# Kernel optimization log

Hardware: AMD Instinct MI355X
Metric: run time of the kernel (lower is better)

## Reference

```python
import jax, jax.numpy as jnp
import numpy as np

N, E = 100000, 600000
IN, H = 164, 128
NH = 4  # attention heads over embed_dim H//4 = 32


def layer_norm(x, g, b, eps=1e-5):
    m = x.mean(-1, keepdims=True)
    v = x.var(-1, keepdims=True)
    return (x - m) * jax.lax.rsqrt(v + eps) * g + b


def gcn_conv(x, W, b, src, dst, n):
    # PyG GCNConv: add self-loops, symmetric D^{-1/2}(A+I)D^{-1/2} normalization.
    deg = jnp.ones((n,), x.dtype).at[dst].add(1.0)  # degree of A+I on target nodes
    dinv = jax.lax.rsqrt(deg)
    xw = x @ W  # [n, out]
    msg = xw[src] * (dinv[src] * dinv[dst])[:, None]  # gather + edge-norm
    agg = jax.ops.segment_sum(msg, dst, num_segments=n)  # scatter-add
    agg = agg + xw * (dinv * dinv)[:, None]  # self-loop term
    return agg + b


def mha_seq1(x, Wq, bq, Wk, bk, Wv, bv, Wo, bo):
    # nn.MultiheadAttention with seq_len==1: softmax over a single key -> weights==1.
    dh = x.shape[-1] // NH
    q = (x @ Wq + bq).reshape(-1, NH, dh)
    k = (x @ Wk + bk).reshape(-1, NH, dh)
    v = (x @ Wv + bv).reshape(-1, NH, dh)
    scores = jnp.sum(q * k, -1, keepdims=True) / jnp.sqrt(jnp.float32(dh))  # [n,NH,1]
    attn = jax.nn.softmax(scores[..., None], axis=-1)[..., 0]  # all ones, kept for fidelity
    out = (attn * v).reshape(-1, NH * dh)
    return out @ Wo + bo


def setup_inputs() -> dict:
    key = jax.random.key(0)
    ks = jax.random.split(key, 16)

    def kaiming(k, i, o):
        return jax.random.normal(k, (i, o), jnp.float32) * (2.0 / i) ** 0.5

    Ha, Hb, Hc = H, H // 2, H // 4  # 128, 64, 32
    return {
        "x": jax.random.normal(ks[0], (N, IN), jnp.float32),
        "edge_index": jax.random.randint(ks[1], (2, E), 0, N),
        "Wi": kaiming(ks[2], IN, Ha), "bi": jnp.zeros((Ha,), jnp.float32),
        "g1": jnp.ones((Ha,), jnp.float32), "b1": jnp.zeros((Ha,), jnp.float32),
        "Wg1": kaiming(ks[3], Ha, Ha), "bg1": jnp.zeros((Ha,), jnp.float32),
        "Wg2": kaiming(ks[4], Ha, Hb), "bg2": jnp.zeros((Hb,), jnp.float32),
        "g2": jnp.ones((Hb,), jnp.float32), "b2": jnp.zeros((Hb,), jnp.float32),
        "Wg3": kaiming(ks[5], Hb, Hc), "bg3": jnp.zeros((Hc,), jnp.float32),
        "Wq": kaiming(ks[6], Hc, Hc), "bq": jnp.zeros((Hc,), jnp.float32),
        "Wk": kaiming(ks[7], Hc, Hc), "bk": jnp.zeros((Hc,), jnp.float32),
        "Wv": kaiming(ks[8], Hc, Hc), "bv": jnp.zeros((Hc,), jnp.float32),
        "Wo": kaiming(ks[9], Hc, Hc), "bo": jnp.zeros((Hc,), jnp.float32),
        "Wc1": kaiming(ks[10], Hc, H // 8), "bc1": jnp.zeros((H // 8,), jnp.float32),
        "Wc2": kaiming(ks[11], H // 8, 32), "bc2": jnp.zeros((32,), jnp.float32),
        "Wc3": kaiming(ks[12], 32, 1), "bc3": jnp.zeros((1,), jnp.float32),
    }


def reference(x, edge_index, Wi, bi, g1, b1, Wg1, bg1, Wg2, bg2, g2, b2,
              Wg3, bg3, Wq, bq, Wk, bk, Wv, bv, Wo, bo,
              Wc1, bc1, Wc2, bc2, Wc3, bc3):
    src, dst = edge_index[0], edge_index[1]
    n = x.shape[0]
    # dropout layers are identity in eval mode
    h = layer_norm(jax.nn.relu(x @ Wi + bi), g1, b1)
    h1 = jax.nn.relu(gcn_conv(h, Wg1, bg1, src, dst, n)) + h
    h2 = layer_norm(jax.nn.relu(gcn_conv(h1, Wg2, bg2, src, dst, n)), g2, b2)
    h3 = jax.nn.relu(gcn_conv(h2, Wg3, bg3, src, dst, n))
    h3 = mha_seq1(h3, Wq, bq, Wk, bk, Wv, bv, Wo, bo)
    h3 = jax.nn.relu(h3 @ Wc1 + bc1)
    h3 = jax.nn.relu(h3 @ Wc2 + bc2)
    return (h3 @ Wc3 + bc3)[:, 0]
```

## Files before the change

kernel.cpp:

```cpp
#include <hip/hip_runtime.h>


typedef __attribute__((ext_vector_type(8))) _Float16 f16x8;
typedef __attribute__((ext_vector_type(4))) _Float16 f16x4;
typedef __attribute__((ext_vector_type(4))) float f32x4;

#define GLOAD_LDS16(gp, lp)                                        \
  __builtin_amdgcn_global_load_lds(                                \
      (const __attribute__((address_space(1))) void*)(gp),         \
      (__attribute__((address_space(3))) void*)(lp), 16, 0, 0)

static __device__ __forceinline__ void wait_vm0() {
  asm volatile("s_waitcnt vmcnt(0)" ::: "memory");
}
static __device__ __forceinline__ void wait_vm1() {
  asm volatile("s_waitcnt vmcnt(1)" ::: "memory");
}
static __device__ __forceinline__ void wait_vm2() {
  asm volatile("s_waitcnt vmcnt(2)" ::: "memory");
}

__global__ void k_count(const int* __restrict__ dst, int* __restrict__ counts, int e) {
  int i = blockIdx.x * blockDim.x + threadIdx.x;
  if (i < e) atomicAdd(&counts[dst[i]], 1);
}

__global__ __launch_bounds__(256) void k_scan_part(
    const int* __restrict__ counts, int* __restrict__ bsums, int n) {
  int tid = threadIdx.x;
  int i0 = blockIdx.x * 1024 + tid * 4;
  int s = 0;
#pragma unroll
  for (int k = 0; k < 4; k++) { int i = i0 + k; if (i < n) s += counts[i]; }
#pragma unroll
  for (int d = 1; d < 64; d <<= 1) s += __shfl_xor(s, d);
  __shared__ int wsum[4];
  int lane = tid & 63, w = tid >> 6;
  if (lane == 0) wsum[w] = s;
  __syncthreads();
  if (tid == 0) bsums[blockIdx.x] = wsum[0] + wsum[1] + wsum[2] + wsum[3];
}

__global__ __launch_bounds__(128) void k_scan_top(int* __restrict__ bsums, int nb) {
  int tid = threadIdx.x;
  int orig = (tid < nb) ? bsums[tid] : 0;
  int v = orig;
  int lane = tid & 63, w = tid >> 6;
#pragma unroll
  for (int d = 1; d < 64; d <<= 1) { int t = __shfl_up(v, d); if (lane >= d) v += t; }
  __shared__ int ws[2];
  if (lane == 63) ws[w] = v;
  __syncthreads();
  if (w == 1) v += ws[0];
  if (tid < nb) bsums[tid] = v - orig;
}

__global__ __launch_bounds__(256) void k_scan_down(
    int* __restrict__ counts, const int* __restrict__ bsums,
    int* __restrict__ offsets, float* __restrict__ dinv, int n, int e) {
  int tid = threadIdx.x;
  int i0 = blockIdx.x * 1024 + tid * 4;
  int c[4]; int tsum = 0;
#pragma unroll
  for (int k = 0; k < 4; k++) { int i = i0 + k; c[k] = (i < n) ? counts[i] : 0; tsum += c[k]; }
  int v = tsum;
  int lane = tid & 63, w = tid >> 6;
#pragma unroll
  for (int d = 1; d < 64; d <<= 1) { int t = __shfl_up(v, d); if (lane >= d) v += t; }
  __shared__ int wsum[4];
  if (lane == 63) wsum[w] = v;
  __syncthreads();
  int wadd = 0;
#pragma unroll
  for (int q = 0; q < 4; q++) if (q < w) wadd += wsum[q];
  int run = (v - tsum) + wadd + bsums[blockIdx.x];
#pragma unroll
  for (int k = 0; k < 4; k++) {
    int i = i0 + k;
    if (i < n) {
      offsets[i] = run;
      dinv[i] = rsqrtf((float)(c[k] + 1));
      counts[i] = 0;
    }
    run += c[k];
  }
  if (blockIdx.x == 0 && tid == 0) offsets[n] = e;
}

__global__ void k_fill(const int* __restrict__ src, const int* __restrict__ dst,
                       const int* __restrict__ offsets, int* __restrict__ cursor,
                       const float* __restrict__ dinv, int2* __restrict__ csr, int e) {
  int i = blockIdx.x * blockDim.x + threadIdx.x;
  if (i >= e) return;
  int s = src[i], d = dst[i];
  int pos = atomicAdd(&cursor[d], 1);
  csr[offsets[d] + pos] = make_int2(s, __float_as_int(dinv[s] * dinv[d]));
}

__device__ __forceinline__ void pack_hi(const float* __restrict__ W,
                                        _Float16* __restrict__ dst,
                                        int K, int N, int u) {
  int lane = u & 63; int rest = u >> 6; int CT = N >> 4;
  int ct = rest % CT, ks = rest / CT;
  int gcol = ct * 16 + (lane & 15);
  int gk0 = ks * 32 + (lane >> 4) * 8;
  size_t o = (size_t)(ks * CT + ct) * 512 + lane * 8;
#pragma unroll
  for (int i = 0; i < 8; i++) {
    float v = (gk0 + i < K) ? W[(size_t)(gk0 + i) * N + gcol] : 0.0f;
    dst[o + i] = (_Float16)v;
  }
}

__global__ void k_setup(const float* __restrict__ Wi, const float* __restrict__ Wg1,
                        const float* __restrict__ Wg2, const float* __restrict__ Wg3,
                        _Float16* __restrict__ pWi, _Float16* __restrict__ pWg1,
                        _Float16* __restrict__ pWg2, _Float16* __restrict__ pWg3,
                        int* __restrict__ counts, float* __restrict__ zp, int n) {
  int b = blockIdx.x;
  if (b < 25) {
    int t = b * 256 + threadIdx.x;
    if (t < 3072) pack_hi(Wi, pWi, 164, 128, t);
    else if (t < 5120) pack_hi(Wg1, pWg1, 128, 128, t - 3072);
    else if (t < 6144) pack_hi(Wg2, pWg2, 128, 64, t - 5120);
    else if (t < 6400) pack_hi(Wg3, pWg3, 64, 32, t - 6144);
  } else {
    if (b == 25 && threadIdx.x < 64) zp[threadIdx.x] = 0.0f;
    int i = (b - 25) * 256 + threadIdx.x;
    if (i < n) counts[i] = 0;
  }
}

__global__ __launch_bounds__(512, 4) void k_gemm_in(
    const float* __restrict__ x, const _Float16* __restrict__ pB,
    const float* __restrict__ bias, const float* __restrict__ gamma,
    const float* __restrict__ beta, const float* __restrict__ zp,
    _Float16* __restrict__ out, int n) {
  constexpr int N = 128, CT = 8;
  __shared__ __align__(16) float sAi[8][2][512];
  int tid = threadIdx.x;
  int lane = tid & 63, w = tid >> 6;
  int rowbase = blockIdx.x * 128 + w * 16;
  const f16x8* Bf = (const f16x8*)pB;

  auto stage = [&](int ks, int buf) {
#pragma unroll
    for (int j = 0; j < 2; j++) {
      int r_ = j * 8 + (lane >> 3);
      int c_ = (lane & 7) ^ (lane >> 3);
      int rg = rowbase + r_;
      bool ok = (rg < n) && (ks < 5 || c_ == 0);
      const void* s = ok ? (const void*)(x + (size_t)rg * 164 + ks * 32 + c_ * 4)
                         : (const void*)zp;
      GLOAD_LDS16(s, &sAi[w][buf][j * 256]);
    }
  };

  f32x4 acc[CT];
#pragma unroll
  for (int c = 0; c < CT; c++) acc[c] = (f32x4)0.0f;

  int rr = lane & 15;
  int c0 = (lane >> 4) * 2;
  int s0 = c0 ^ (rr & 7);
  int s1 = (c0 + 1) ^ (rr & 7);

  stage(0, 0);
#pragma unroll
  for (int ks = 0; ks < 6; ks++) {
    f16x8 bfr[CT];
#pragma unroll
    for (int c = 0; c < CT; c++) bfr[c] = Bf[(ks * CT + c) * 64 + lane];
    if (ks + 1 < 6) { stage(ks + 1, (ks + 1) & 1); wait_vm2(); }
    else wait_vm0();
    const float* bp = &sAi[w][ks & 1][0];
    float4 u0 = *(const float4*)&bp[rr * 32 + s0 * 4];
    float4 u1 = *(const float4*)&bp[rr * 32 + s1 * 4];
    float v[8] = {u0.x, u0.y, u0.z, u0.w, u1.x, u1.y, u1.z, u1.w};
    f16x8 ah, al;
#pragma unroll
    for (int i = 0; i < 8; i++) {
      ah[i] = (_Float16)v[i];
      al[i] = (_Float16)(v[i] - (float)ah[i]);
    }
#pragma unroll
    for (int c = 0; c < CT; c++) {
      acc[c] = __builtin_amdgcn_mfma_f32_16x16x32_f16(ah, bfr[c], acc[c], 0, 0, 0);
      acc[c] = __builtin_amdgcn_mfma_f32_16x16x32_f16(al, bfr[c], acc[c], 0, 0, 0);
    }
  }

  int r0 = (lane >> 4) * 4;
  int li = lane & 15;
  float s1v[4] = {0, 0, 0, 0}, s2v[4] = {0, 0, 0, 0};
#pragma unroll
  for (int c = 0; c < CT; c++) {
    float bb = bias[c * 16 + li];
#pragma unroll
    for (int r = 0; r < 4; r++) {
      float t = acc[c][r] + bb;
      t = t > 0.0f ? t : 0.0f;
      acc[c][r] = t;
      s1v[r] += t;
      s2v[r] += t * t;
    }
  }
#pragma unroll
  for (int m = 1; m < 16; m <<= 1) {
#pragma unroll
    for (int r = 0; r < 4; r++) {
      s1v[r] += __shfl_xor(s1v[r], m);
      s2v[r] += __shfl_xor(s2v[r], m);
    }
  }
#pragma unroll
  for (int c = 0; c < CT; c++) {
    float gv = gamma[c * 16 + li], bv = beta[c * 16 + li];
#pragma unroll
    for (int r = 0; r < 4; r++) {
      int node = rowbase + r0 + r;
      if (node < n) {
        float mean = s1v[r] * (1.0f / N);
        float var = s2v[r] * (1.0f / N) - mean * mean;
        float rs = rsqrtf(var + 1e-5f);
        out[(size_t)node * N + c * 16 + li] =
            (_Float16)((acc[c][r] - mean) * rs * gv + bv);
      }
    }
  }
}

template <int K, int N>
__global__ __launch_bounds__(512, 4) void k_gemm_f16(
    const _Float16* __restrict__ A, const _Float16* __restrict__ pB,
    const float* __restrict__ zp, _Float16* __restrict__ out, int n) {
  constexpr int KS = K / 32, CT = N / 16;
  __shared__ __align__(16) _Float16 sA[8][2][512];
  int tid = threadIdx.x;
  int lane = tid & 63, w = tid >> 6;
  int rowbase = blockIdx.x * 128 + w * 16;
  const f16x8* Bf = (const f16x8*)pB;

  int r_ = lane >> 2;
  int c_ = (lane & 3) ^ (r_ & 3);
  int rg = rowbase + r_;
  const _Float16* asrc = A + (size_t)rg * K + c_ * 8;
  bool rok = rg < n;

  auto stage = [&](int ks, int buf) {
    const void* s = rok ? (const void*)(asrc + ks * 32) : (const void*)zp;
    GLOAD_LDS16(s, &sA[w][buf][0]);
  };

  f32x4 acc[CT];
#pragma unroll
  for (int c = 0; c < CT; c++) acc[c] = (f32x4)0.0f;

  int rr = lane & 15;
  int slot = (lane >> 4) ^ (rr & 3);

  stage(0, 0);
#pragma unroll
  for (int ks = 0; ks < KS; ks++) {
    f16x8 bfr[CT];
#pragma unroll
    for (int c = 0; c < CT; c++) bfr[c] = Bf[(ks * CT + c) * 64 + lane];
    if (ks + 1 < KS) { stage(ks + 1, (ks + 1) & 1); wait_vm1(); }
    else wait_vm0();
    f16x8 av = *(const f16x8*)&sA[w][ks & 1][rr * 32 + slot * 8];
#pragma unroll
    for (int c = 0; c < CT; c++) {
      acc[c] = __builtin_amdgcn_mfma_f32_16x16x32_f16(av, bfr[c], acc[c], 0, 0, 0);
    }
  }

  int r0 = (lane >> 4) * 4;
  int li = lane & 15;
#pragma unroll
  for (int c = 0; c < CT; c++) {
#pragma unroll
    for (int r = 0; r < 4; r++) {
      int node = rowbase + r0 + r;
      if (node < n) out[(size_t)node * N + c * 16 + li] = (_Float16)acc[c][r];
    }
  }
}

template <int OUT_D, int MODE>
__global__ __launch_bounds__(256, 2) void k_gather(
    const int* __restrict__ off, const int2* __restrict__ csr,
    const _Float16* __restrict__ xw, const float* __restrict__ dinv,
    const float* __restrict__ bias, const _Float16* __restrict__ auxh,
    const float* __restrict__ gamma, const float* __restrict__ beta,
    _Float16* __restrict__ out, int n) {
  constexpr int TPN = OUT_D / 4;
  constexpr int NPB = 256 / TPN;
  int tid = threadIdx.x;
  int node = blockIdx.x * NPB + tid / TPN;
  int li = tid % TPN;
  if (node >= n) return;
  int start = off[node], end = off[node + 1];
  float di = dinv[node];
  float d2 = di * di;
  const _Float16* xp = xw + 4 * li;
  f16x4 self = *(const f16x4*)(xp + (size_t)node * OUT_D);
  f16x4 hres;
  if constexpr (MODE == 0)
    hres = *(const f16x4*)(auxh + (size_t)node * OUT_D + 4 * li);
  float a0 = (float)self[0] * d2 + bias[4 * li + 0];
  float a1 = (float)self[1] * d2 + bias[4 * li + 1];
  float a2 = (float)self[2] * d2 + bias[4 * li + 2];
  float a3 = (float)self[3] * d2 + bias[4 * li + 3];
  for (int cb = start; cb < end; cb += TPN) {
    int m = end - cb; if (m > TPN) m = TPN;
    int sv = node; float nv = 0.0f;
    if (li < m) { int2 me = csr[cb + li]; sv = me.x; nv = __int_as_float(me.y); }
    for (int j0 = 0; j0 < m; j0 += 8) {
      int s0 = __shfl(sv, j0 + 0, TPN), s1 = __shfl(sv, j0 + 1, TPN);
      int s2 = __shfl(sv, j0 + 2, TPN), s3 = __shfl(sv, j0 + 3, TPN);
      int s4 = __shfl(sv, j0 + 4, TPN), s5 = __shfl(sv, j0 + 5, TPN);
      int s6 = __shfl(sv, j0 + 6, TPN), s7 = __shfl(sv, j0 + 7, TPN);
      float w0 = __shfl(nv, j0 + 0, TPN), w1 = __shfl(nv, j0 + 1, TPN);
      float w2 = __shfl(nv, j0 + 2, TPN), w3 = __shfl(nv, j0 + 3, TPN);
      float w4 = __shfl(nv, j0 + 4, TPN), w5 = __shfl(nv, j0 + 5, TPN);
      float w6 = __shfl(nv, j0 + 6, TPN), w7 = __shfl(nv, j0 + 7, TPN);
      f16x4 v0 = *(const f16x4*)(xp + (size_t)s0 * OUT_D);
      f16x4 v1 = *(const f16x4*)(xp + (size_t)s1 * OUT_D);
      f16x4 v2 = *(const f16x4*)(xp + (size_t)s2 * OUT_D);
      f16x4 v3 = *(const f16x4*)(xp + (size_t)s3 * OUT_D);
      f16x4 v4 = *(const f16x4*)(xp + (size_t)s4 * OUT_D);
      f16x4 v5 = *(const f16x4*)(xp + (size_t)s5 * OUT_D);
      f16x4 v6 = *(const f16x4*)(xp + (size_t)s6 * OUT_D);
      f16x4 v7 = *(const f16x4*)(xp + (size_t)s7 * OUT_D);
      a0 += (float)v0[0] * w0 + (float)v1[0] * w1 + (float)v2[0] * w2 + (float)v3[0] * w3
          + (float)v4[0] * w4 + (float)v5[0] * w5 + (float)v6[0] * w6 + (float)v7[0] * w7;
      a1 += (float)v0[1] * w0 + (float)v1[1] * w1 + (float)v2[1] * w2 + (float)v3[1] * w3
          + (float)v4[1] * w4 + (float)v5[1] * w5 + (float)v6[1] * w6 + (float)v7[1] * w7;
      a2 += (float)v0[2] * w0 + (float)v1[2] * w1 + (float)v2[2] * w2 + (float)v3[2] * w3
          + (float)v4[2] * w4 + (float)v5[2] * w5 + (float)v6[2] * w6 + (float)v7[2] * w7;
      a3 += (float)v0[3] * w0 + (float)v1[3] * w1 + (float)v2[3] * w2 + (float)v3[3] * w3
          + (float)v4[3] * w4 + (float)v5[3] * w5 + (float)v6[3] * w6 + (float)v7[3] * w7;
    }
  }
  _Float16* po = out + (size_t)node * OUT_D + 4 * li;
  if constexpr (MODE == 0) {
    f16x4 o;
    o[0] = (_Float16)((a0 > 0.0f ? a0 : 0.0f) + (float)hres[0]);
    o[1] = (_Float16)((a1 > 0.0f ? a1 : 0.0f) + (float)hres[1]);
    o[2] = (_Float16)((a2 > 0.0f ? a2 : 0.0f) + (float)hres[2]);
    o[3] = (_Float16)((a3 > 0.0f ? a3 : 0.0f) + (float)hres[3]);
    *(f16x4*)po = o;
  } else if constexpr (MODE == 1) {
    float v0 = a0 > 0.0f ? a0 : 0.0f, v1 = a1 > 0.0f ? a1 : 0.0f;
    float v2 = a2 > 0.0f ? a2 : 0.0f, v3 = a3 > 0.0f ? a3 : 0.0f;
    float s1 = v0 + v1 + v2 + v3;
    float s2 = v0 * v0 + v1 * v1 + v2 * v2 + v3 * v3;
#pragma unroll
    for (int d = 1; d < TPN; d <<= 1) {
      s1 += __shfl_xor(s1, d, TPN);
      s2 += __shfl_xor(s2, d, TPN);
    }
    float m_ = s1 * (1.0f / OUT_D);
    float var = s2 * (1.0f / OUT_D) - m_ * m_;
    float rs = rsqrtf(var + 1e-5f);
    f16x4 o;
    o[0] = (_Float16)((v0 - m_) * rs * gamma[4 * li + 0] + beta[4 * li + 0]);
    o[1] = (_Float16)((v1 - m_) * rs * gamma[4 * li + 1] + beta[4 * li + 1]);
    o[2] = (_Float16)((v2 - m_) * rs * gamma[4 * li + 2] + beta[4 * li + 2]);
    o[3] = (_Float16)((v3 - m_) * rs * gamma[4 * li + 3] + beta[4 * li + 3]);
    *(f16x4*)po = o;
  } else {
    f16x4 o;
    o[0] = (_Float16)a0; o[1] = (_Float16)a1;
    o[2] = (_Float16)a2; o[3] = (_Float16)a3;
    *(f16x4*)po = o;
  }
}

__global__ __launch_bounds__(256) void k_tail(
    const _Float16* __restrict__ agg3, const float* __restrict__ Wv,
    const float* __restrict__ bv, const float* __restrict__ Wo,
    const float* __restrict__ bo, const float* __restrict__ Wc1,
    const float* __restrict__ bc1, const float* __restrict__ Wc2,
    const float* __restrict__ bc2, const float* __restrict__ Wc3,
    const float* __restrict__ bc3, float* __restrict__ out, int n) {
  __shared__ float sWv[1024], sWo[1024], sWc1[512], sWc2[512];
  __shared__ float sbv[32], sbo[32], sbc2[32], sWc3[32], sbc1[16], sbc3[1];
  int tid = threadIdx.x;
  for (int i = tid; i < 1024; i += 256) { sWv[i] = Wv[i]; sWo[i] = Wo[i]; }
  for (int i = tid; i < 512; i += 256) { sWc1[i] = Wc1[i]; sWc2[i] = Wc2[i]; }
  if (tid < 32) { sbv[tid] = bv[tid]; sbo[tid] = bo[tid];
                  sbc2[tid] = bc2[tid]; sWc3[tid] = Wc3[tid]; }
  if (tid < 16) sbc1[tid] = bc1[tid];
  if (tid == 0) sbc3[0] = bc3[0];
  __syncthreads();
  int node = blockIdx.x * blockDim.x + tid;
  if (node >= n) return;
  float a[32];
  const f16x8* row8 = (const f16x8*)(agg3 + (size_t)node * 32);
#pragma unroll
  for (int q = 0; q < 4; q++) {
    f16x8 t = row8[q];
#pragma unroll
    for (int i = 0; i < 8; i++) {
      float f = (float)t[i];
      a[8 * q + i] = f > 0.0f ? f : 0.0f;
    }
  }
  float v[32];
#pragma unroll
  for (int j = 0; j < 32; j++) v[j] = sbv[j];
  for (int k = 0; k < 32; k++) {
#pragma unroll
    for (int j = 0; j < 32; j++) v[j] += a[k] * sWv[k * 32 + j];
  }
  float o[32];
#pragma unroll
  for (int j = 0; j < 32; j++) o[j] = sbo[j];
  for (int k = 0; k < 32; k++) {
#pragma unroll
    for (int j = 0; j < 32; j++) o[j] += v[k] * sWo[k * 32 + j];
  }
  float c1[16];
#pragma unroll
  for (int j = 0; j < 16; j++) c1[j] = sbc1[j];
  for (int k = 0; k < 32; k++) {
#pragma unroll
    for (int j = 0; j < 16; j++) c1[j] += o[k] * sWc1[k * 16 + j];
  }
#pragma unroll
  for (int j = 0; j < 16; j++) c1[j] = c1[j] > 0.0f ? c1[j] : 0.0f;
  float c2[32];
#pragma unroll
  for (int j = 0; j < 32; j++) c2[j] = sbc2[j];
  for (int k = 0; k < 16; k++) {
#pragma unroll
    for (int j = 0; j < 32; j++) c2[j] += c1[k] * sWc2[k * 32 + j];
  }
  float r = sbc3[0];
#pragma unroll
  for (int k = 0; k < 32; k++) {
    float c = c2[k] > 0.0f ? c2[k] : 0.0f;
    r += c * sWc3[k];
  }
  out[node] = r;
}

extern "C" void kernel_launch(void* const* d_in, const int* in_sizes, int n_in,
                              void* d_out, int out_size, void* d_ws, size_t ws_size,
                              hipStream_t stream) {
  const float* x   = (const float*)d_in[0];
  const int* ei    = (const int*)d_in[1];
  const float* Wi  = (const float*)d_in[2];
  const float* bi  = (const float*)d_in[3];
  const float* g1  = (const float*)d_in[4];
  const float* b1  = (const float*)d_in[5];
  const float* Wg1 = (const float*)d_in[6];
  const float* bg1 = (const float*)d_in[7];
  const float* Wg2 = (const float*)d_in[8];
  const float* bg2 = (const float*)d_in[9];
  const float* g2  = (const float*)d_in[10];
  const float* b2  = (const float*)d_in[11];
  const float* Wg3 = (const float*)d_in[12];
  const float* bg3 = (const float*)d_in[13];
  const float* Wv  = (const float*)d_in[18];
  const float* bv  = (const float*)d_in[19];
  const float* Wo  = (const float*)d_in[20];
  const float* bo  = (const float*)d_in[21];
  const float* Wc1 = (const float*)d_in[22];
  const float* bc1 = (const float*)d_in[23];
  const float* Wc2 = (const float*)d_in[24];
  const float* bc2 = (const float*)d_in[25];
  const float* Wc3 = (const float*)d_in[26];
  const float* bc3 = (const float*)d_in[27];

  const int n = in_sizes[0] / 164;
  const int e = in_sizes[1] / 2;
  const int* src = ei;
  const int* dst = ei + e;

  char* ws = (char*)d_ws;
  size_t off = 0;
  auto alloc = [&](size_t bytes) {
    char* p = ws + off;
    off += (bytes + 255) & ~(size_t)255;
    return p;
  };
  _Float16* A     = (_Float16*)alloc((size_t)n * 128 * 2);
  _Float16* B     = (_Float16*)alloc((size_t)n * 128 * 2);
  _Float16* C     = (_Float16*)alloc((size_t)n * 128 * 2);
  float* dinv     = (float*)alloc((size_t)n * 4);
  int*   counts   = (int*)alloc((size_t)n * 4);
  int*   offsets  = (int*)alloc((size_t)(n + 1) * 4);
  int*   bsums    = (int*)alloc(128 * 4);
  int2*  csr      = (int2*)alloc((size_t)e * 8);
  _Float16* pWi   = (_Float16*)alloc(3072 * 16);
  _Float16* pWg1  = (_Float16*)alloc(2048 * 16);
  _Float16* pWg2  = (_Float16*)alloc(1024 * 16);
  _Float16* pWg3  = (_Float16*)alloc(256 * 16);
  float* zp       = (float*)alloc(64 * 4);
  (void)ws_size;

  const int BS = 256;
  const int SB = (n + 1023) / 1024;
  const int GB = (n + 127) / 128;

  k_setup<<<25 + (n + 255) / 256, 256, 0, stream>>>(
      Wi, Wg1, Wg2, Wg3, pWi, pWg1, pWg2, pWg3, counts, zp, n);

  k_count<<<(e + BS - 1) / BS, BS, 0, stream>>>(dst, counts, e);
  k_scan_part<<<SB, 256, 0, stream>>>(counts, bsums, n);
  k_scan_top<<<1, 128, 0, stream>>>(bsums, SB);
  k_scan_down<<<SB, 256, 0, stream>>>(counts, bsums, offsets, dinv, n, e);
  k_fill<<<(e + BS - 1) / BS, BS, 0, stream>>>(src, dst, offsets, counts, dinv,
                                               csr, e);

  k_gemm_in<<<GB, 512, 0, stream>>>(x, pWi, bi, g1, b1, zp, A, n);

  k_gemm_f16<128, 128><<<GB, 512, 0, stream>>>(A, pWg1, zp, B, n);
  k_gather<128, 0><<<(n + 7) / 8, 256, 0, stream>>>(
      offsets, csr, B, dinv, bg1, A, nullptr, nullptr, C, n);

  k_gemm_f16<128, 64><<<GB, 512, 0, stream>>>(C, pWg2, zp, A, n);
  k_gather<64, 1><<<(n + 15) / 16, 256, 0, stream>>>(
      offsets, csr, A, dinv, bg2, nullptr, g2, b2, B, n);

  k_gemm_f16<64, 32><<<GB, 512, 0, stream>>>(B, pWg3, zp, A, n);
  k_gather<32, 2><<<(n + 31) / 32, 256, 0, stream>>>(
      offsets, csr, A, dinv, bg3, nullptr, nullptr, nullptr, C, n);

  k_tail<<<(n + BS - 1) / BS, BS, 0, stream>>>(
      C, Wv, bv, Wo, bo, Wc1, bc1, Wc2, bc2, Wc3, bc3, (float*)d_out, n);
}
```

Baseline: 227.4 us.

## Fuse final gather into tail, merge scan stages, stage GEMM outputs via LDS, drop split-f16

Several changes at once. The final GCN gather is fused into the MLP tail kernel through an LDS tile, which removes one launch and the f16 round trip of the aggregated features. The top-level scan kernel is dropped, and each scan_down block now sums its own prefix of block sums. The GEMM epilogues are staged through LDS so global stores become coalesced 16-byte writes. The input GEMM also drops the hi/lo f16 split, which halves its MFMAs but lowers input precision to plain f16.

```diff
diff --git a/kernel.cpp b/kernel.cpp
--- a/kernel.cpp
+++ b/kernel.cpp
@@ -18,6 +18,10 @@
 }
 static __device__ __forceinline__ void wait_vm2() {
   asm volatile("s_waitcnt vmcnt(2)" ::: "memory");
+}
+static __device__ __forceinline__ void wait_lgkm0() {
+  asm volatile("s_waitcnt lgkmcnt(0)" ::: "memory");
+  __builtin_amdgcn_sched_barrier(0);
 }
 
 __global__ void k_count(const int* __restrict__ dst, int* __restrict__ counts, int e) {
@@ -41,39 +45,32 @@
   if (tid == 0) bsums[blockIdx.x] = wsum[0] + wsum[1] + wsum[2] + wsum[3];
 }
 
-__global__ __launch_bounds__(128) void k_scan_top(int* __restrict__ bsums, int nb) {
-  int tid = threadIdx.x;
-  int orig = (tid < nb) ? bsums[tid] : 0;
-  int v = orig;
-  int lane = tid & 63, w = tid >> 6;
-#pragma unroll
-  for (int d = 1; d < 64; d <<= 1) { int t = __shfl_up(v, d); if (lane >= d) v += t; }
-  __shared__ int ws[2];
-  if (lane == 63) ws[w] = v;
-  __syncthreads();
-  if (w == 1) v += ws[0];
-  if (tid < nb) bsums[tid] = v - orig;
-}
-
 __global__ __launch_bounds__(256) void k_scan_down(
     int* __restrict__ counts, const int* __restrict__ bsums,
-    int* __restrict__ offsets, float* __restrict__ dinv, int n, int e) {
+    int* __restrict__ offsets, float* __restrict__ dinv, int n, int e, int nb) {
   int tid = threadIdx.x;
+  int lane = tid & 63, w = tid >> 6;
+  __shared__ int wsum[4], psum[4];
+  int pv = (tid < nb && tid < blockIdx.x) ? bsums[tid] : 0;
+#pragma unroll
+  for (int d = 1; d < 64; d <<= 1) pv += __shfl_xor(pv, d);
+  if (lane == 0) psum[w] = pv;
+  __syncthreads();
+  int blockpref = psum[0] + psum[1] + psum[2] + psum[3];
+
   int i0 = blockIdx.x * 1024 + tid * 4;
   int c[4]; int tsum = 0;
 #pragma unroll
   for (int k = 0; k < 4; k++) { int i = i0 + k; c[k] = (i < n) ? counts[i] : 0; tsum += c[k]; }
   int v = tsum;
-  int lane = tid & 63, w = tid >> 6;
 #pragma unroll
   for (int d = 1; d < 64; d <<= 1) { int t = __shfl_up(v, d); if (lane >= d) v += t; }
-  __shared__ int wsum[4];
   if (lane == 63) wsum[w] = v;
   __syncthreads();
   int wadd = 0;
 #pragma unroll
   for (int q = 0; q < 4; q++) if (q < w) wadd += wsum[q];
-  int run = (v - tsum) + wadd + bsums[blockIdx.x];
+  int run = (v - tsum) + wadd + blockpref;
 #pragma unroll
   for (int k = 0; k < 4; k++) {
     int i = i0 + k;
@@ -177,17 +174,12 @@
     float4 u0 = *(const float4*)&bp[rr * 32 + s0 * 4];
     float4 u1 = *(const float4*)&bp[rr * 32 + s1 * 4];
     float v[8] = {u0.x, u0.y, u0.z, u0.w, u1.x, u1.y, u1.z, u1.w};
-    f16x8 ah, al;
-#pragma unroll
-    for (int i = 0; i < 8; i++) {
-      ah[i] = (_Float16)v[i];
-      al[i] = (_Float16)(v[i] - (float)ah[i]);
-    }
-#pragma unroll
-    for (int c = 0; c < CT; c++) {
+    f16x8 ah;
+#pragma unroll
+    for (int i = 0; i < 8; i++) ah[i] = (_Float16)v[i];
+#pragma unroll
+    for (int c = 0; c < CT; c++)
       acc[c] = __builtin_amdgcn_mfma_f32_16x16x32_f16(ah, bfr[c], acc[c], 0, 0, 0);
-      acc[c] = __builtin_amdgcn_mfma_f32_16x16x32_f16(al, bfr[c], acc[c], 0, 0, 0);
-    }
   }
 
   int r0 = (lane >> 4) * 4;
@@ -213,20 +205,29 @@
       s2v[r] += __shfl_xor(s2v[r], m);
     }
   }
+  wait_lgkm0();
+  _Float16* lr = (_Float16*)&sAi[w][0][0];
 #pragma unroll
   for (int c = 0; c < CT; c++) {
     float gv = gamma[c * 16 + li], bv = beta[c * 16 + li];
 #pragma unroll
     for (int r = 0; r < 4; r++) {
-      int node = rowbase + r0 + r;
-      if (node < n) {
-        float mean = s1v[r] * (1.0f / N);
-        float var = s2v[r] * (1.0f / N) - mean * mean;
-        float rs = rsqrtf(var + 1e-5f);
-        out[(size_t)node * N + c * 16 + li] =
-            (_Float16)((acc[c][r] - mean) * rs * gv + bv);
-      }
-    }
+      float mean = s1v[r] * (1.0f / N);
+      float var = s2v[r] * (1.0f / N) - mean * mean;
+      float rs = rsqrtf(var + 1e-5f);
+      lr[(r0 + r) * 128 + c * 16 + li] =
+          (_Float16)((acc[c][r] - mean) * rs * gv + bv);
+    }
+  }
+  wait_lgkm0();
+#pragma unroll
+  for (int i = 0; i < 4; i++) {
+    int chunk = i * 64 + lane;
+    int rloc = chunk >> 4;
+    int cc = chunk & 15;
+    if (rowbase + rloc < n)
+      *(f16x8*)&out[(size_t)(rowbase + rloc) * 128 + cc * 8] =
+          *(const f16x8*)&lr[chunk * 8];
   }
 }
 
@@ -236,6 +237,7 @@
     const float* __restrict__ zp, _Float16* __restrict__ out, int n) {
   constexpr int KS = K / 32, CT = N / 16;
   __shared__ __align__(16) _Float16 sA[8][2][512];
+  __shared__ __align__(16) _Float16 sR[8][16 * N];
   int tid = threadIdx.x;
   int lane = tid & 63, w = tid >> 6;
   int rowbase = blockIdx.x * 128 + w * 16;
@@ -269,20 +271,29 @@
     else wait_vm0();
     f16x8 av = *(const f16x8*)&sA[w][ks & 1][rr * 32 + slot * 8];
 #pragma unroll
-    for (int c = 0; c < CT; c++) {
+    for (int c = 0; c < CT; c++)
       acc[c] = __builtin_amdgcn_mfma_f32_16x16x32_f16(av, bfr[c], acc[c], 0, 0, 0);
-    }
   }
 
   int r0 = (lane >> 4) * 4;
   int li = lane & 15;
+  wait_lgkm0();
+  _Float16* lr = &sR[w][0];
 #pragma unroll
   for (int c = 0; c < CT; c++) {
 #pragma unroll
-    for (int r = 0; r < 4; r++) {
-      int node = rowbase + r0 + r;
-      if (node < n) out[(size_t)node * N + c * 16 + li] = (_Float16)acc[c][r];
-    }
+    for (int r = 0; r < 4; r++)
+      lr[(r0 + r) * N + c * 16 + li] = (_Float16)acc[c][r];
+  }
+  wait_lgkm0();
+#pragma unroll
+  for (int i = 0; i < N / 32; i++) {
+    int chunk = i * 64 + lane;
+    int rloc = chunk / (N / 8);
+    int cc = chunk % (N / 8);
+    if (rowbase + rloc < n)
+      *(f16x8*)&out[(size_t)(rowbase + rloc) * N + cc * 8] =
+          *(const f16x8*)&lr[chunk * 8];
   }
 }
 
@@ -350,7 +361,7 @@
     o[2] = (_Float16)((a2 > 0.0f ? a2 : 0.0f) + (float)hres[2]);
     o[3] = (_Float16)((a3 > 0.0f ? a3 : 0.0f) + (float)hres[3]);
     *(f16x4*)po = o;
-  } else if constexpr (MODE == 1) {
+  } else {
     float v0 = a0 > 0.0f ? a0 : 0.0f, v1 = a1 > 0.0f ? a1 : 0.0f;
     float v2 = a2 > 0.0f ? a2 : 0.0f, v3 = a3 > 0.0f ? a3 : 0.0f;
     float s1 = v0 + v1 + v2 + v3;
@@ -369,21 +380,19 @@
     o[2] = (_Float16)((v2 - m_) * rs * gamma[4 * li + 2] + beta[4 * li + 2]);
     o[3] = (_Float16)((v3 - m_) * rs * gamma[4 * li + 3] + beta[4 * li + 3]);
     *(f16x4*)po = o;
-  } else {
-    f16x4 o;
-    o[0] = (_Float16)a0; o[1] = (_Float16)a1;
-    o[2] = (_Float16)a2; o[3] = (_Float16)a3;
-    *(f16x4*)po = o;
-  }
-}
-
-__global__ __launch_bounds__(256) void k_tail(
-    const _Float16* __restrict__ agg3, const float* __restrict__ Wv,
+  }
+}
+
+__global__ __launch_bounds__(256, 2) void k_gt(
+    const int* __restrict__ off, const int2* __restrict__ csr,
+    const _Float16* __restrict__ xw, const float* __restrict__ dinv,
+    const float* __restrict__ bg3, const float* __restrict__ Wv,
     const float* __restrict__ bv, const float* __restrict__ Wo,
     const float* __restrict__ bo, const float* __restrict__ Wc1,
     const float* __restrict__ bc1, const float* __restrict__ Wc2,
     const float* __restrict__ bc2, const float* __restrict__ Wc3,
     const float* __restrict__ bc3, float* __restrict__ out, int n) {
+  __shared__ float sAgg[256][33];
   __shared__ float sWv[1024], sWo[1024], sWc1[512], sWc2[512];
   __shared__ float sbv[32], sbo[32], sbc2[32], sWc3[32], sbc1[16], sbc3[1];
   int tid = threadIdx.x;
@@ -393,19 +402,65 @@
                   sbc2[tid] = bc2[tid]; sWc3[tid] = Wc3[tid]; }
   if (tid < 16) sbc1[tid] = bc1[tid];
   if (tid == 0) sbc3[0] = bc3[0];
+
+  int base0 = blockIdx.x * 256;
+  int li = tid & 7;
+  const _Float16* xp = xw + 4 * li;
+  for (int sub = 0; sub < 8; sub++) {
+    int nl = sub * 32 + (tid >> 3);
+    int node = base0 + nl;
+    if (node < n) {
+      int start = off[node], end = off[node + 1];
+      float di = dinv[node];
+      float d2 = di * di;
+      f16x4 self = *(const f16x4*)(xp + (size_t)node * 32);
+      float a0 = (float)self[0] * d2 + bg3[4 * li + 0];
+      float a1 = (float)self[1] * d2 + bg3[4 * li + 1];
+      float a2 = (float)self[2] * d2 + bg3[4 * li + 2];
+      float a3 = (float)self[3] * d2 + bg3[4 * li + 3];
+      for (int cb = start; cb < end; cb += 8) {
+        int m = end - cb; if (m > 8) m = 8;
+        int sv = node; float nv = 0.0f;
+        if (li < m) { int2 me = csr[cb + li]; sv = me.x; nv = __int_as_float(me.y); }
+        for (int j0 = 0; j0 < m; j0 += 8) {
+          int s0 = __shfl(sv, j0 + 0, 8), s1 = __shfl(sv, j0 + 1, 8);
+          int s2 = __shfl(sv, j0 + 2, 8), s3 = __shfl(sv, j0 + 3, 8);
+          int s4 = __shfl(sv, j0 + 4, 8), s5 = __shfl(sv, j0 + 5, 8);
+          int s6 = __shfl(sv, j0 + 6, 8), s7 = __shfl(sv, j0 + 7, 8);
+          float w0 = __shfl(nv, j0 + 0, 8), w1 = __shfl(nv, j0 + 1, 8);
+          float w2 = __shfl(nv, j0 + 2, 8), w3 = __shfl(nv, j0 + 3, 8);
+          float w4 = __shfl(nv, j0 + 4, 8), w5 = __shfl(nv, j0 + 5, 8);
+          float w6 = __shfl(nv, j0 + 6, 8), w7 = __shfl(nv, j0 + 7, 8);
+          f16x4 v0 = *(const f16x4*)(xp + (size_t)s0 * 32);
+          f16x4 v1 = *(const f16x4*)(xp + (size_t)s1 * 32);
+          f16x4 v2 = *(const f16x4*)(xp + (size_t)s2 * 32);
+          f16x4 v3 = *(const f16x4*)(xp + (size_t)s3 * 32);
+          f16x4 v4 = *(const f16x4*)(xp + (size_t)s4 * 32);
+          f16x4 v5 = *(const f16x4*)(xp + (size_t)s5 * 32);
+          f16x4 v6 = *(const f16x4*)(xp + (size_t)s6 * 32);
+          f16x4 v7 = *(const f16x4*)(xp + (size_t)s7 * 32);
+          a0 += (float)v0[0] * w0 + (float)v1[0] * w1 + (float)v2[0] * w2 + (float)v3[0] * w3
+              + (float)v4[0] * w4 + (float)v5[0] * w5 + (float)v6[0] * w6 + (float)v7[0] * w7;
+          a1 += (float)v0[1] * w0 + (float)v1[1] * w1 + (float)v2[1] * w2 + (float)v3[1] * w3
+              + (float)v4[1] * w4 + (float)v5[1] * w5 + (float)v6[1] * w6 + (float)v7[1] * w7;
+          a2 += (float)v0[2] * w0 + (float)v1[2] * w1 + (float)v2[2] * w2 + (float)v3[2] * w3
+              + (float)v4[2] * w4 + (float)v5[2] * w5 + (float)v6[2] * w6 + (float)v7[2] * w7;
+          a3 += (float)v0[3] * w0 + (float)v1[3] * w1 + (float)v2[3] * w2 + (float)v3[3] * w3
+              + (float)v4[3] * w4 + (float)v5[3] * w5 + (float)v6[3] * w6 + (float)v7[3] * w7;
+        }
+      }
+      float* dst = &sAgg[nl][4 * li];
+      dst[0] = a0; dst[1] = a1; dst[2] = a2; dst[3] = a3;
+    }
+  }
   __syncthreads();
-  int node = blockIdx.x * blockDim.x + tid;
+  int node = base0 + tid;
   if (node >= n) return;
   float a[32];
-  const f16x8* row8 = (const f16x8*)(agg3 + (size_t)node * 32);
-#pragma unroll
-  for (int q = 0; q < 4; q++) {
-    f16x8 t = row8[q];
-#pragma unroll
-    for (int i = 0; i < 8; i++) {
-      float f = (float)t[i];
-      a[8 * q + i] = f > 0.0f ? f : 0.0f;
-    }
+#pragma unroll
+  for (int j = 0; j < 32; j++) {
+    float f = sAgg[tid][j];
+    a[j] = f > 0.0f ? f : 0.0f;
   }
   float v[32];
 #pragma unroll
@@ -492,7 +547,7 @@
   float* dinv     = (float*)alloc((size_t)n * 4);
   int*   counts   = (int*)alloc((size_t)n * 4);
   int*   offsets  = (int*)alloc((size_t)(n + 1) * 4);
-  int*   bsums    = (int*)alloc(128 * 4);
+  int*   bsums    = (int*)alloc(256 * 4);
   int2*  csr      = (int2*)alloc((size_t)e * 8);
   _Float16* pWi   = (_Float16*)alloc(3072 * 16);
   _Float16* pWg1  = (_Float16*)alloc(2048 * 16);
@@ -510,8 +565,7 @@
 
   k_count<<<(e + BS - 1) / BS, BS, 0, stream>>>(dst, counts, e);
   k_scan_part<<<SB, 256, 0, stream>>>(counts, bsums, n);
-  k_scan_top<<<1, 128, 0, stream>>>(bsums, SB);
-  k_scan_down<<<SB, 256, 0, stream>>>(counts, bsums, offsets, dinv, n, e);
+  k_scan_down<<<SB, 256, 0, stream>>>(counts, bsums, offsets, dinv, n, e, SB);
   k_fill<<<(e + BS - 1) / BS, BS, 0, stream>>>(src, dst, offsets, counts, dinv,
                                                csr, e);
 
@@ -526,9 +580,7 @@
       offsets, csr, A, dinv, bg2, nullptr, g2, b2, B, n);
 
   k_gemm_f16<64, 32><<<GB, 512, 0, stream>>>(B, pWg3, zp, A, n);
-  k_gather<32, 2><<<(n + 31) / 32, 256, 0, stream>>>(
-      offsets, csr, A, dinv, bg3, nullptr, nullptr, nullptr, C, n);
-
-  k_tail<<<(n + BS - 1) / BS, BS, 0, stream>>>(
-      C, Wv, bv, Wo, bo, Wc1, bc1, Wc2, bc2, Wc3, bc3, (float*)d_out, n);
-}
+  k_gt<<<(n + 255) / 256, 256, 0, stream>>>(
+      offsets, csr, A, dinv, bg3, Wv, bv, Wo, bo, Wc1, bc1, Wc2, bc2,
+      Wc3, bc3, (float*)d_out, n);
+}
```

After: 219.1 us. -3.7%, faster.

## Prefetch B fragments, stage GEMM outputs via LDS, drop split-fp16 and scan_top

Applied to the files above, without the earlier changes.

Several changes land together. The GEMM kernels now double-buffer the B weight fragments in registers, one k-step ahead, and adjust the vmcnt waits to match. Outputs are written through LDS as 16-byte row-contiguous stores instead of scattered 2-byte stores. The scan kernel is dropped: each scan_down block now sums the partial sums of the blocks before it itself. Separately, k_gemm_in stops using the hi/lo fp16 split for x, halving its MFMAs at the cost of fp32 input precision.

```diff
diff --git a/kernel.cpp b/kernel.cpp
--- a/kernel.cpp
+++ b/kernel.cpp
@@ -13,11 +13,18 @@
 static __device__ __forceinline__ void wait_vm0() {
   asm volatile("s_waitcnt vmcnt(0)" ::: "memory");
 }
-static __device__ __forceinline__ void wait_vm1() {
-  asm volatile("s_waitcnt vmcnt(1)" ::: "memory");
-}
-static __device__ __forceinline__ void wait_vm2() {
-  asm volatile("s_waitcnt vmcnt(2)" ::: "memory");
+static __device__ __forceinline__ void wait_vm10() {
+  asm volatile("s_waitcnt vmcnt(10)" ::: "memory");
+}
+static __device__ __forceinline__ void wait_vm5() {
+  asm volatile("s_waitcnt vmcnt(5)" ::: "memory");
+}
+static __device__ __forceinline__ void wait_vm3() {
+  asm volatile("s_waitcnt vmcnt(3)" ::: "memory");
+}
+static __device__ __forceinline__ void wait_lgkm0() {
+  asm volatile("s_waitcnt lgkmcnt(0)" ::: "memory");
+  __builtin_amdgcn_sched_barrier(0);
 }
 
 __global__ void k_count(const int* __restrict__ dst, int* __restrict__ counts, int e) {
@@ -41,39 +48,32 @@
   if (tid == 0) bsums[blockIdx.x] = wsum[0] + wsum[1] + wsum[2] + wsum[3];
 }
 
-__global__ __launch_bounds__(128) void k_scan_top(int* __restrict__ bsums, int nb) {
-  int tid = threadIdx.x;
-  int orig = (tid < nb) ? bsums[tid] : 0;
-  int v = orig;
-  int lane = tid & 63, w = tid >> 6;
-#pragma unroll
-  for (int d = 1; d < 64; d <<= 1) { int t = __shfl_up(v, d); if (lane >= d) v += t; }
-  __shared__ int ws[2];
-  if (lane == 63) ws[w] = v;
-  __syncthreads();
-  if (w == 1) v += ws[0];
-  if (tid < nb) bsums[tid] = v - orig;
-}
-
 __global__ __launch_bounds__(256) void k_scan_down(
     int* __restrict__ counts, const int* __restrict__ bsums,
-    int* __restrict__ offsets, float* __restrict__ dinv, int n, int e) {
+    int* __restrict__ offsets, float* __restrict__ dinv, int n, int e, int nb) {
   int tid = threadIdx.x;
+  int lane = tid & 63, w = tid >> 6;
+  __shared__ int wsum[4], psum[4];
+  int pv = (tid < nb && tid < blockIdx.x) ? bsums[tid] : 0;
+#pragma unroll
+  for (int d = 1; d < 64; d <<= 1) pv += __shfl_xor(pv, d);
+  if (lane == 0) psum[w] = pv;
+  __syncthreads();
+  int blockpref = psum[0] + psum[1] + psum[2] + psum[3];
+
   int i0 = blockIdx.x * 1024 + tid * 4;
   int c[4]; int tsum = 0;
 #pragma unroll
   for (int k = 0; k < 4; k++) { int i = i0 + k; c[k] = (i < n) ? counts[i] : 0; tsum += c[k]; }
   int v = tsum;
-  int lane = tid & 63, w = tid >> 6;
 #pragma unroll
   for (int d = 1; d < 64; d <<= 1) { int t = __shfl_up(v, d); if (lane >= d) v += t; }
-  __shared__ int wsum[4];
   if (lane == 63) wsum[w] = v;
   __syncthreads();
   int wadd = 0;
 #pragma unroll
   for (int q = 0; q < 4; q++) if (q < w) wadd += wsum[q];
-  int run = (v - tsum) + wadd + bsums[blockIdx.x];
+  int run = (v - tsum) + wadd + blockpref;
 #pragma unroll
   for (int k = 0; k < 4; k++) {
     int i = i0 + k;
@@ -136,7 +136,7 @@
     const float* __restrict__ bias, const float* __restrict__ gamma,
     const float* __restrict__ beta, const float* __restrict__ zp,
     _Float16* __restrict__ out, int n) {
-  constexpr int N = 128, CT = 8;
+  constexpr int N = 128, CT = 8, KS = 6;
   __shared__ __align__(16) float sAi[8][2][512];
   int tid = threadIdx.x;
   int lane = tid & 63, w = tid >> 6;
@@ -165,29 +165,32 @@
   int s0 = c0 ^ (rr & 7);
   int s1 = (c0 + 1) ^ (rr & 7);
 
+  f16x8 bfr[2][CT];
+#pragma unroll
+  for (int c = 0; c < CT; c++) bfr[0][c] = Bf[c * 64 + lane];
   stage(0, 0);
-#pragma unroll
-  for (int ks = 0; ks < 6; ks++) {
-    f16x8 bfr[CT];
-#pragma unroll
-    for (int c = 0; c < CT; c++) bfr[c] = Bf[(ks * CT + c) * 64 + lane];
-    if (ks + 1 < 6) { stage(ks + 1, (ks + 1) & 1); wait_vm2(); }
-    else wait_vm0();
+
+#pragma unroll
+  for (int ks = 0; ks < KS; ks++) {
+    if (ks + 1 < KS) {
+#pragma unroll
+      for (int c = 0; c < CT; c++)
+        bfr[(ks + 1) & 1][c] = Bf[((ks + 1) * CT + c) * 64 + lane];
+      stage(ks + 1, (ks + 1) & 1);
+      wait_vm10();
+    } else {
+      wait_vm0();
+    }
     const float* bp = &sAi[w][ks & 1][0];
     float4 u0 = *(const float4*)&bp[rr * 32 + s0 * 4];
     float4 u1 = *(const float4*)&bp[rr * 32 + s1 * 4];
     float v[8] = {u0.x, u0.y, u0.z, u0.w, u1.x, u1.y, u1.z, u1.w};
-    f16x8 ah, al;
-#pragma unroll
-    for (int i = 0; i < 8; i++) {
-      ah[i] = (_Float16)v[i];
-      al[i] = (_Float16)(v[i] - (float)ah[i]);
-    }
-#pragma unroll
-    for (int c = 0; c < CT; c++) {
-      acc[c] = __builtin_amdgcn_mfma_f32_16x16x32_f16(ah, bfr[c], acc[c], 0, 0, 0);
-      acc[c] = __builtin_amdgcn_mfma_f32_16x16x32_f16(al, bfr[c], acc[c], 0, 0, 0);
-    }
+    f16x8 ah;
+#pragma unroll
+    for (int i = 0; i < 8; i++) ah[i] = (_Float16)v[i];
+#pragma unroll
+    for (int c = 0; c < CT; c++)
+      acc[c] = __builtin_amdgcn_mfma_f32_16x16x32_f16(ah, bfr[ks & 1][c], acc[c], 0, 0, 0);
   }
 
   int r0 = (lane >> 4) * 4;
@@ -213,20 +216,29 @@
       s2v[r] += __shfl_xor(s2v[r], m);
     }
   }
+  wait_lgkm0();
+  _Float16* lr = (_Float16*)&sAi[w][0][0];
 #pragma unroll
   for (int c = 0; c < CT; c++) {
     float gv = gamma[c * 16 + li], bv = beta[c * 16 + li];
 #pragma unroll
     for (int r = 0; r < 4; r++) {
-      int node = rowbase + r0 + r;
-      if (node < n) {
-        float mean = s1v[r] * (1.0f / N);
-        float var = s2v[r] * (1.0f / N) - mean * mean;
-        float rs = rsqrtf(var + 1e-5f);
-        out[(size_t)node * N + c * 16 + li] =
-            (_Float16)((acc[c][r] - mean) * rs * gv + bv);
-      }
-    }
+      float mean = s1v[r] * (1.0f / N);
+      float var = s2v[r] * (1.0f / N) - mean * mean;
+      float rs = rsqrtf(var + 1e-5f);
+      lr[(r0 + r) * 128 + c * 16 + li] =
+          (_Float16)((acc[c][r] - mean) * rs * gv + bv);
+    }
+  }
+  wait_lgkm0();
+#pragma unroll
+  for (int i = 0; i < 4; i++) {
+    int chunk = i * 64 + lane;
+    int rloc = chunk >> 4;
+    int cc = chunk & 15;
+    if (rowbase + rloc < n)
+      *(f16x8*)&out[(size_t)(rowbase + rloc) * 128 + cc * 8] =
+          *(const f16x8*)&lr[chunk * 8];
   }
 }
 
@@ -236,6 +248,7 @@
     const float* __restrict__ zp, _Float16* __restrict__ out, int n) {
   constexpr int KS = K / 32, CT = N / 16;
   __shared__ __align__(16) _Float16 sA[8][2][512];
+  __shared__ __align__(16) _Float16 sR[8][16 * N];
   int tid = threadIdx.x;
   int lane = tid & 63, w = tid >> 6;
   int rowbase = blockIdx.x * 128 + w * 16;
@@ -259,30 +272,47 @@
   int rr = lane & 15;
   int slot = (lane >> 4) ^ (rr & 3);
 
+  f16x8 bfr[2][CT];
+#pragma unroll
+  for (int c = 0; c < CT; c++) bfr[0][c] = Bf[c * 64 + lane];
   stage(0, 0);
+
 #pragma unroll
   for (int ks = 0; ks < KS; ks++) {
-    f16x8 bfr[CT];
-#pragma unroll
-    for (int c = 0; c < CT; c++) bfr[c] = Bf[(ks * CT + c) * 64 + lane];
-    if (ks + 1 < KS) { stage(ks + 1, (ks + 1) & 1); wait_vm1(); }
-    else wait_vm0();
+    if (ks + 1 < KS) {
+#pragma unroll
+      for (int c = 0; c < CT; c++)
+        bfr[(ks + 1) & 1][c] = Bf[((ks + 1) * CT + c) * 64 + lane];
+      stage(ks + 1, (ks + 1) & 1);
+      if (CT == 8) wait_vm10(); else if (CT == 4) wait_vm5(); else wait_vm3();
+    } else {
+      wait_vm0();
+    }
     f16x8 av = *(const f16x8*)&sA[w][ks & 1][rr * 32 + slot * 8];
 #pragma unroll
-    for (int c = 0; c < CT; c++) {
-      acc[c] = __builtin_amdgcn_mfma_f32_16x16x32_f16(av, bfr[c], acc[c], 0, 0, 0);
-    }
+    for (int c = 0; c < CT; c++)
+      acc[c] = __builtin_amdgcn_mfma_f32_16x16x32_f16(av, bfr[ks & 1][c], acc[c], 0, 0, 0);
   }
 
   int r0 = (lane >> 4) * 4;
   int li = lane & 15;
+  wait_lgkm0();
+  _Float16* lr = &sR[w][0];
 #pragma unroll
   for (int c = 0; c < CT; c++) {
 #pragma unroll
-    for (int r = 0; r < 4; r++) {
-      int node = rowbase + r0 + r;
-      if (node < n) out[(size_t)node * N + c * 16 + li] = (_Float16)acc[c][r];
-    }
+    for (int r = 0; r < 4; r++)
+      lr[(r0 + r) * N + c * 16 + li] = (_Float16)acc[c][r];
+  }
+  wait_lgkm0();
+#pragma unroll
+  for (int i = 0; i < N / 32; i++) {
+    int chunk = i * 64 + lane;
+    int rloc = chunk / (N / 8);
+    int cc = chunk % (N / 8);
+    if (rowbase + rloc < n)
+      *(f16x8*)&out[(size_t)(rowbase + rloc) * N + cc * 8] =
+          *(const f16x8*)&lr[chunk * 8];
   }
 }
 
@@ -492,7 +522,7 @@
   float* dinv     = (float*)alloc((size_t)n * 4);
   int*   counts   = (int*)alloc((size_t)n * 4);
   int*   offsets  = (int*)alloc((size_t)(n + 1) * 4);
-  int*   bsums    = (int*)alloc(128 * 4);
+  int*   bsums    = (int*)alloc(256 * 4);
   int2*  csr      = (int2*)alloc((size_t)e * 8);
   _Float16* pWi   = (_Float16*)alloc(3072 * 16);
   _Float16* pWg1  = (_Float16*)alloc(2048 * 16);
@@ -510,8 +540,7 @@
 
   k_count<<<(e + BS - 1) / BS, BS, 0, stream>>>(dst, counts, e);
   k_scan_part<<<SB, 256, 0, stream>>>(counts, bsums, n);
-  k_scan_top<<<1, 128, 0, stream>>>(bsums, SB);
-  k_scan_down<<<SB, 256, 0, stream>>>(counts, bsums, offsets, dinv, n, e);
+  k_scan_down<<<SB, 256, 0, stream>>>(counts, bsums, offsets, dinv, n, e, SB);
   k_fill<<<(e + BS - 1) / BS, BS, 0, stream>>>(src, dst, offsets, counts, dinv,
                                                csr, e);
 
```

Result: faster. 213.8 us (-6.0%).
